# Optimization experiments

Measured on AMD Instinct MI355X. Metric: run time of the kernel, lower is better.

Reference implementation:

```python
import jax, jax.numpy as jnp
import numpy as np

N_NODES = 80000
N_EDGES = 1280000
IN_CH = 128
HID = 64
N_GRAPHS = 64
DROPOUT_P = 0.3


def setup_inputs() -> dict:
    key = jax.random.key(0)
    ks = jax.random.split(key, 12)
    x = jax.random.normal(ks[0], (N_NODES, IN_CH), dtype=jnp.float32)
    edge_index = jax.random.randint(ks[1], (2, N_EDGES), 0, N_NODES, dtype=jnp.int64 if jax.config.read('jax_enable_x64') else jnp.int32)
    batch = jnp.sort(jax.random.randint(ks[2], (N_NODES,), 0, N_GRAPHS))
    def lin(k, fan_in, fan_out):
        lim = 1.0 / np.sqrt(fan_in)
        kw, kb = jax.random.split(k)
        W = jax.random.uniform(kw, (fan_in, fan_out), minval=-lim, maxval=lim, dtype=jnp.float32)
        b = jax.random.uniform(kb, (fan_out,), minval=-lim, maxval=lim, dtype=jnp.float32)
        return W, b
    W1, b1 = lin(ks[3], IN_CH, HID)
    W2, b2 = lin(ks[4], HID, HID)
    W3, b3 = lin(ks[5], HID, HID)
    Wm1, bm1 = lin(ks[6], HID, HID)
    Wm2, bm2 = lin(ks[7], HID, 1)
    return {"x": x, "edge_index": edge_index, "batch": batch,
            "W1": W1, "b1": b1, "W2": W2, "b2": b2, "W3": W3, "b3": b3,
            "Wm1": Wm1, "bm1": bm1, "Wm2": Wm2, "bm2": bm2}


def _gcn_conv(x, W, b, src, dst, deg_inv_sqrt):
    # PyG GCNConv: h = X W; add self-loops; norm_e = d^-1/2[src] * d^-1/2[dst]
    h = x @ W  # [N, F]
    norm = deg_inv_sqrt[src] * deg_inv_sqrt[dst]  # [E]
    agg = jax.ops.segment_sum(h[src] * norm[:, None], dst, num_segments=x.shape[0])
    agg = agg + h * (deg_inv_sqrt * deg_inv_sqrt)[:, None]  # self-loop term d^-1
    return agg + b


def _dropout(x, key, p):
    keep = jax.random.bernoulli(key, 1.0 - p, x.shape)
    return jnp.where(keep, x / (1.0 - p), 0.0)


def reference(x, edge_index, batch, W1, b1, W2, b2, W3, b3, Wm1, bm1, Wm2, bm2):
    src, dst = edge_index[0], edge_index[1]
    N = x.shape[0]
    # in-degree on dst, +1 for self-loop (PyG default normalization)
    deg = jax.ops.segment_sum(jnp.ones_like(dst, dtype=x.dtype), dst, num_segments=N) + 1.0
    deg_inv_sqrt = jax.lax.rsqrt(deg)

    dk = jax.random.split(jax.random.key(42), 4)
    h = _dropout(jax.nn.relu(_gcn_conv(x, W1, b1, src, dst, deg_inv_sqrt)), dk[0], DROPOUT_P)
    h = _dropout(jax.nn.relu(_gcn_conv(h, W2, b2, src, dst, deg_inv_sqrt)), dk[1], DROPOUT_P)
    h = _dropout(jax.nn.relu(_gcn_conv(h, W3, b3, src, dst, deg_inv_sqrt)), dk[2], DROPOUT_P)

    # global mean pool per graph
    sums = jax.ops.segment_sum(h, batch, num_segments=N_GRAPHS)
    counts = jax.ops.segment_sum(jnp.ones((N,), dtype=h.dtype), batch, num_segments=N_GRAPHS)
    pooled = sums / jnp.maximum(counts, 1.0)[:, None]  # [G, HID]

    # MLP head: Linear -> ReLU -> Dropout -> Linear
    m = jax.nn.relu(pooled @ Wm1 + bm1)
    m = _dropout(m, dk[3], DROPOUT_P)
    return m @ Wm2 + bm2  # [G, 1]
```

## Files before the change

### kernel.cpp

```cpp
#include <hip/hip_runtime.h>
#include <hip/hip_fp8.h>
#include <stdint.h>

#define HID 64
#define INCH 128
#define NGRAPH 64
#define KEEPP 0.7f
#define CAP 64
#define CAPSH 6
#define BD 16

typedef __attribute__((ext_vector_type(8))) short short8;
typedef __attribute__((ext_vector_type(4))) float floatx4;

__device__ __forceinline__ uint8_t f2e4(float f) {
  __hip_fp8_e4m3 t(f);
  return (uint8_t)t.__x;
}
__device__ __forceinline__ float e42f(uint8_t b) {
  __hip_fp8_e4m3 t;
  t.__x = (__hip_fp8_storage_t)b;
  return (float)t;
}
__device__ __forceinline__ ushort f2bf(float v) {
  uint32_t u = __float_as_uint(v);
  return (ushort)((u + 0x7FFFu + ((u >> 16) & 1u)) >> 16);
}
__device__ __forceinline__ float bf2f(ushort b) {
  return __uint_as_float((uint32_t)b << 16);
}

__host__ __device__ inline void tf2x32(uint32_t k0, uint32_t k1,
                                       uint32_t& x0, uint32_t& x1) {
  const uint32_t ks2 = k0 ^ k1 ^ 0x1BD11BDAu;
#define ROTL32(v, d) (((v) << (d)) | ((v) >> (32 - (d))))
#define TF_RND(r) { x0 += x1; x1 = ROTL32(x1, r); x1 ^= x0; }
  x0 += k0; x1 += k1;
  TF_RND(13) TF_RND(15) TF_RND(26) TF_RND(6)
  x0 += k1;  x1 += ks2 + 1u;
  TF_RND(17) TF_RND(29) TF_RND(16) TF_RND(24)
  x0 += ks2; x1 += k0 + 2u;
  TF_RND(13) TF_RND(15) TF_RND(26) TF_RND(6)
  x0 += k0;  x1 += k1 + 3u;
  TF_RND(17) TF_RND(29) TF_RND(16) TF_RND(24)
  x0 += k1;  x1 += ks2 + 4u;
  TF_RND(13) TF_RND(15) TF_RND(26) TF_RND(6)
  x0 += ks2; x1 += k0 + 5u;
#undef TF_RND
#undef ROTL32
}

__device__ __forceinline__ bool keep_mask(uint32_t k0, uint32_t k1, uint32_t idx) {
  uint32_t x0 = 0u, x1 = idx;
  tf2x32(k0, k1, x0, x1);
  uint32_t bits = x0 ^ x1;
  float u = __uint_as_float((bits >> 9) | 0x3f800000u) - 1.0f;
  return u < KEEPP;
}

__device__ __forceinline__ void wsplit_one(const float* __restrict__ W,
                                           short8* __restrict__ Wh,
                                           short8* __restrict__ Wl, int i) {
  int lane = i & 63, f = i >> 6;
  int kc = f >> 2, ct = f & 3;
  int kbase = kc * 32 + ((lane >> 4) << 3);
  int n = ct * 16 + (lane & 15);
  short8 h, l;
#pragma unroll
  for (int j = 0; j < 8; ++j) {
    float w = W[(size_t)(kbase + j) * HID + n];
    uint32_t u = __float_as_uint(w);
    h[j] = (short)(u >> 16);
    float r = w - __uint_as_float(u & 0xFFFF0000u);
    l[j] = (short)(__float_as_uint(r) >> 16);
  }
  Wh[i] = h;
  Wl[i] = l;
}

__global__ __launch_bounds__(256) void k_w1(const float* __restrict__ W1,
                                            short8* __restrict__ Wh1,
                                            short8* __restrict__ Wl1) {
  wsplit_one(W1, Wh1, Wl1, blockIdx.x * 256 + (int)threadIdx.x);
}

template <int K, int OUTMODE>
__device__ __forceinline__ void mgemm_tile(const float* __restrict__ A,
                                           const short8* __restrict__ Wh,
                                           const short8* __restrict__ Wl,
                                           uint8_t* __restrict__ C,
                                           const int* __restrict__ counts,
                                           int N, int tile) {
  constexpr int KC = K / 32;
  const int lane = threadIdx.x & 63;
  const int wv = threadIdx.x >> 6;
  const int m = lane & 15;
  const int q = lane >> 4;
  const int row0 = tile * 64 + wv * 16;
  if (row0 >= N) return;
  const int arow = min(row0 + m, N - 1);
  const float* __restrict__ ap = A + (size_t)arow * K + (q << 3);

  floatx4 acc[4];
#pragma unroll
  for (int ct = 0; ct < 4; ++ct) acc[ct] = (floatx4){0.f, 0.f, 0.f, 0.f};

#pragma unroll
  for (int kc = 0; kc < KC; ++kc) {
    const floatx4* apv = (const floatx4*)(ap + kc * 32);
    floatx4 x0 = apv[0];
    floatx4 x1 = apv[1];
    short8 ah, al;
#pragma unroll
    for (int j = 0; j < 4; ++j) {
      uint32_t u = __float_as_uint(x0[j]);
      ah[j] = (short)(u >> 16);
      float r = x0[j] - __uint_as_float(u & 0xFFFF0000u);
      al[j] = (short)(__float_as_uint(r) >> 16);
    }
#pragma unroll
    for (int j = 0; j < 4; ++j) {
      uint32_t u = __float_as_uint(x1[j]);
      ah[4 + j] = (short)(u >> 16);
      float r = x1[j] - __uint_as_float(u & 0xFFFF0000u);
      al[4 + j] = (short)(__float_as_uint(r) >> 16);
    }
#pragma unroll
    for (int ct = 0; ct < 4; ++ct) {
      short8 bh = Wh[(kc * 4 + ct) * 64 + lane];
      short8 bl = Wl[(kc * 4 + ct) * 64 + lane];
      acc[ct] = __builtin_amdgcn_mfma_f32_16x16x32_bf16(ah, bh, acc[ct], 0, 0, 0);
      acc[ct] = __builtin_amdgcn_mfma_f32_16x16x32_bf16(ah, bl, acc[ct], 0, 0, 0);
      acc[ct] = __builtin_amdgcn_mfma_f32_16x16x32_bf16(al, bh, acc[ct], 0, 0, 0);
    }
  }

  if (OUTMODE == 0) {
    ushort* __restrict__ cp = (ushort*)C + (size_t)row0 * HID;
#pragma unroll
    for (int ct = 0; ct < 4; ++ct)
#pragma unroll
      for (int r = 0; r < 4; ++r) {
        int rr = (q << 2) + r;
        if (row0 + rr < N) cp[(size_t)rr * HID + ct * 16 + m] = f2bf(acc[ct][r]);
      }
  } else {
    float dv[4];
#pragma unroll
    for (int r = 0; r < 4; ++r) {
      int gr = min(row0 + (q << 2) + r, N - 1);
      dv[r] = rsqrtf((float)counts[gr] + 1.0f);
    }
    uint8_t* __restrict__ cp = C + (size_t)row0 * HID;
#pragma unroll
    for (int ct = 0; ct < 4; ++ct)
#pragma unroll
      for (int r = 0; r < 4; ++r) {
        int rr = (q << 2) + r;
        if (row0 + rr < N) cp[(size_t)rr * HID + ct * 16 + m] = f2e4(acc[ct][r] * dv[r]);
      }
  }
}

template <int K>
__global__ __launch_bounds__(256) void k_build_gemm(
    const float* __restrict__ A, const short8* __restrict__ Wh,
    const short8* __restrict__ Wl, uint8_t* __restrict__ C, int N,
    const int* __restrict__ src, const int* __restrict__ dst,
    int* __restrict__ counts, int* __restrict__ cap,
    int E, int build_blocks, int gemm_blocks,
    const float* __restrict__ W2, short8* __restrict__ Wh2, short8* __restrict__ Wl2,
    const float* __restrict__ W3, short8* __restrict__ Wh3, short8* __restrict__ Wl3,
    const int* __restrict__ batch, int* __restrict__ gends) {
  const int TB = build_blocks + gemm_blocks;
  const int tid = (int)threadIdx.x;
  if ((int)blockIdx.x >= TB) {
    int xb = (int)blockIdx.x - TB;
    if (xb < 2) {
      wsplit_one(W2, Wh2, Wl2, xb * 256 + tid);
    } else if (xb < 4) {
      wsplit_one(W3, Wh3, Wl3, (xb - 2) * 256 + tid);
    } else {
      int bi = xb - 4;
      for (int i = bi * 256 + tid; i < N; i += BD * 256) {
        int g = batch[i];
        int gn = (i + 1 < N) ? batch[i + 1] : -1;
        if (g != gn) gends[g] = i + 1;
      }
    }
    return;
  }
  const long T = (long)TB;
  const long b = (long)blockIdx.x;
  const long gb = (b * gemm_blocks) / T;
  const bool is_g = (((b + 1) * gemm_blocks) / T) != gb;
  if (!is_g) {
    int bb = (int)(b - gb);
    int e = bb * 256 + tid;
    if (e < E) {
      int s = src[e], d = dst[e];
      int r = atomicAdd(&counts[d], 1);
      if (r < CAP) cap[(d << CAPSH) + r] = s;
    }
    return;
  }
  mgemm_tile<K, 0>(A, Wh, Wl, C, nullptr, N, (int)gb);
}

template <int K>
__global__ __launch_bounds__(256) void k_mgemm_s(const float* __restrict__ A,
                                                 const short8* __restrict__ Wh,
                                                 const short8* __restrict__ Wl,
                                                 uint8_t* __restrict__ C,
                                                 const int* __restrict__ counts,
                                                 int N) {
  mgemm_tile<K, 1>(A, Wh, Wl, C, counts, N, (int)blockIdx.x);
}

__global__ __launch_bounds__(256) void k_scale(const ushort* __restrict__ Bh,
                                               const int* __restrict__ counts,
                                               uint8_t* __restrict__ B0, int N) {
  int t = blockIdx.x * 256 + threadIdx.x;
  int total = N * (HID / 8);
  if (t >= total) return;
  int node = t >> 3;
  float dn = rsqrtf((float)counts[node] + 1.0f);
  const ushort* ip = Bh + (size_t)t * 8;
  ushort4 a = *(const ushort4*)ip;
  ushort4 b = *(const ushort4*)(ip + 4);
  uint8_t o[8];
  o[0] = f2e4(bf2f(a.x) * dn); o[1] = f2e4(bf2f(a.y) * dn);
  o[2] = f2e4(bf2f(a.z) * dn); o[3] = f2e4(bf2f(a.w) * dn);
  o[4] = f2e4(bf2f(b.x) * dn); o[5] = f2e4(bf2f(b.y) * dn);
  o[6] = f2e4(bf2f(b.z) * dn); o[7] = f2e4(bf2f(b.w) * dn);
  *(uint2*)(B0 + (size_t)t * 8) = *(uint2*)o;
}

__global__ __launch_bounds__(256) void k_gather_s(const uint8_t* __restrict__ tmp,
                                                  const int* __restrict__ counts,
                                                  const int* __restrict__ cap,
                                                  const float* __restrict__ bias,
                                                  float* __restrict__ outh, int N,
                                                  uint32_t k0, uint32_t k1) {
  const int node = blockIdx.x * 4 + (threadIdx.x >> 6);
  const int lane = threadIdx.x & 63;
  if (node >= N) return;
  const int degn = __builtin_amdgcn_readfirstlane(counts[node]);
  const int deg = min(degn, CAP);
  const int base = node << CAPSH;
  const int idx = node * HID + lane;
  const float selfv = e42f(tmp[idx]);
  const float blane = bias[lane];
  float acc0 = 0.0f, acc1 = 0.0f, acc2 = 0.0f, acc3 = 0.0f;
  int j = 0;
  for (; j + 7 < deg; j += 8) {
    int4 e0 = *(const int4*)&cap[base + j];
    int4 e1 = *(const int4*)&cap[base + j + 4];
    float v0 = e42f(tmp[(size_t)e0.x * HID + lane]);
    float v1 = e42f(tmp[(size_t)e0.y * HID + lane]);
    float v2 = e42f(tmp[(size_t)e0.z * HID + lane]);
    float v3 = e42f(tmp[(size_t)e0.w * HID + lane]);
    float v4 = e42f(tmp[(size_t)e1.x * HID + lane]);
    float v5 = e42f(tmp[(size_t)e1.y * HID + lane]);
    float v6 = e42f(tmp[(size_t)e1.z * HID + lane]);
    float v7 = e42f(tmp[(size_t)e1.w * HID + lane]);
    acc0 += v0; acc1 += v1; acc2 += v2; acc3 += v3;
    acc0 += v4; acc1 += v5; acc2 += v6; acc3 += v7;
  }
  for (; j + 1 < deg; j += 2) {
    int2 p = *(const int2*)&cap[base + j];
    acc0 += e42f(tmp[(size_t)p.x * HID + lane]);
    acc1 += e42f(tmp[(size_t)p.y * HID + lane]);
  }
  if (j < deg) {
    int s = cap[base + j];
    acc2 += e42f(tmp[(size_t)s * HID + lane]);
  }
  float acc = (acc0 + acc1) + (acc2 + acc3);
  const float dn = rsqrtf((float)degn + 1.0f);
  float v = dn * (acc + selfv) + blane;
  v = fmaxf(v, 0.0f);
  v = keep_mask(k0, k1, (uint32_t)idx) ? v / KEEPP : 0.0f;
  outh[idx] = v;
}

__global__ __launch_bounds__(256) void k_pool(const float* __restrict__ h,
                                              const int* __restrict__ batch,
                                              float* __restrict__ sums, int N) {
  __shared__ float ls[NGRAPH * HID];
  for (int i = threadIdx.x; i < NGRAPH * HID; i += 256) ls[i] = 0.0f;
  __syncthreads();
  const int lane = threadIdx.x & 63;
  const int wave = threadIdx.x >> 6;
  int per = (N + gridDim.x - 1) / gridDim.x;
  int beg = blockIdx.x * per;
  int end = min(N, beg + per);
  for (int i = beg + wave; i < end; i += 4) {
    int g = batch[i];
    atomicAdd(&ls[g * HID + lane], h[(size_t)i * HID + lane]);
  }
  __syncthreads();
  for (int i = threadIdx.x; i < NGRAPH * HID; i += 256)
    if (ls[i] != 0.0f) atomicAdd(&sums[i], ls[i]);
}

__global__ __launch_bounds__(256) void k_head(const float* __restrict__ sums,
                                              const int* __restrict__ gends,
                                              const float* __restrict__ Wm1,
                                              const float* __restrict__ bm1,
                                              const float* __restrict__ Wm2,
                                              const float* __restrict__ bm2,
                                              float* __restrict__ out,
                                              uint32_t k0, uint32_t k1) {
  __shared__ float cnts_s[NGRAPH];
  __shared__ float pooled[NGRAPH * HID];
  __shared__ float m[NGRAPH * HID];
  if (threadIdx.x < 64) {
    int g = threadIdx.x;
    int e = gends[g];
#pragma unroll
    for (int off = 1; off < 64; off <<= 1) {
      int o = __shfl_up(e, off);
      if (g >= off) e = max(e, o);
    }
    int prev = __shfl_up(e, 1);
    if (g == 0) prev = 0;
    cnts_s[g] = (float)(e - prev);
  }
  __syncthreads();
  for (int i = threadIdx.x; i < NGRAPH * HID; i += 256) {
    int g = i >> 6;
    pooled[i] = sums[i] / fmaxf(cnts_s[g], 1.0f);
  }
  __syncthreads();
  for (int i = threadIdx.x; i < NGRAPH * HID; i += 256) {
    int g = i >> 6, j = i & 63;
    float acc = bm1[j];
#pragma unroll 8
    for (int k = 0; k < HID; ++k)
      acc = fmaf(pooled[g * HID + k], Wm1[k * HID + j], acc);
    acc = fmaxf(acc, 0.0f);
    m[i] = keep_mask(k0, k1, (uint32_t)i) ? acc / KEEPP : 0.0f;
  }
  __syncthreads();
  if (threadIdx.x < NGRAPH) {
    int g = threadIdx.x;
    float acc = bm2[0];
#pragma unroll 8
    for (int j = 0; j < HID; ++j)
      acc = fmaf(m[g * HID + j], Wm2[j], acc);
    out[g] = acc;
  }
}

extern "C" void kernel_launch(void* const* d_in, const int* in_sizes, int n_in,
                              void* d_out, int out_size, void* d_ws, size_t ws_size,
                              hipStream_t stream) {
  const float* x     = (const float*)d_in[0];
  const int*   ei    = (const int*)d_in[1];
  const int*   batch = (const int*)d_in[2];
  const float* W1 = (const float*)d_in[3];
  const float* b1 = (const float*)d_in[4];
  const float* W2 = (const float*)d_in[5];
  const float* b2 = (const float*)d_in[6];
  const float* W3 = (const float*)d_in[7];
  const float* b3 = (const float*)d_in[8];
  const float* Wm1 = (const float*)d_in[9];
  const float* bm1 = (const float*)d_in[10];
  const float* Wm2 = (const float*)d_in[11];
  const float* bm2 = (const float*)d_in[12];
  float* out = (float*)d_out;

  const int N = in_sizes[0] / INCH;
  const int E = in_sizes[1] / 2;
  const int* src = ei;
  const int* dst = ei + E;

  char* ws = (char*)d_ws;
  size_t off = 0;
  uint8_t* B0 = (uint8_t*)(ws + off); off += (size_t)N * HID;
  off = (off + 15) & ~(size_t)15;
  float* B1     = (float*)(ws + off); off += (size_t)N * HID * 4;
  int*   counts = (int*)  (ws + off); off += (size_t)N * 4;
  float* sums   = (float*)(ws + off); off += NGRAPH * HID * 4;
  int*   gends  = (int*)  (ws + off); off += NGRAPH * 4;
  int*   cap    = (int*)  (ws + off); off += (size_t)N * CAP * 4;
  off = (off + 15) & ~(size_t)15;
  short8* Wh1 = (short8*)(ws + off); off += 1024 * 16;
  short8* Wl1 = (short8*)(ws + off); off += 1024 * 16;
  short8* Wh2 = (short8*)(ws + off); off += 512 * 16;
  short8* Wl2 = (short8*)(ws + off); off += 512 * 16;
  short8* Wh3 = (short8*)(ws + off); off += 512 * 16;
  short8* Wl3 = (short8*)(ws + off); off += 512 * 16;
  ushort* Bh = (ushort*)B1;

  uint32_t dk[4][2];
  for (uint32_t i = 0; i < 4; ++i) {
    uint32_t a = 0u, b = i;
    tf2x32(0u, 42u, a, b);
    dk[i][0] = a; dk[i][1] = b;
  }

  const int build_grid = (E + 255) / 256;
  const int mg_grid    = (N + 63) / 64;
  const int gath_grid  = (N + 3) / 4;
  const int scale_grid = (N * (HID / 8) + 255) / 256;

  hipMemsetAsync(counts, 0, (size_t)N * 4 + NGRAPH * HID * 4 + NGRAPH * 4, stream);
  k_w1<<<4, 256, 0, stream>>>(W1, Wh1, Wl1);

  k_build_gemm<INCH><<<build_grid + mg_grid + 4 + BD, 256, 0, stream>>>(
      x, Wh1, Wl1, (uint8_t*)Bh, N, src, dst, counts, cap, E,
      build_grid, mg_grid, W2, Wh2, Wl2, W3, Wh3, Wl3, batch, gends);
  k_scale<<<scale_grid, 256, 0, stream>>>(Bh, counts, B0, N);
  k_gather_s<<<gath_grid, 256, 0, stream>>>(B0, counts, cap, b1,
                                            B1, N, dk[0][0], dk[0][1]);
  k_mgemm_s<HID><<<mg_grid, 256, 0, stream>>>(B1, Wh2, Wl2, B0, counts, N);
  k_gather_s<<<gath_grid, 256, 0, stream>>>(B0, counts, cap, b2,
                                            B1, N, dk[1][0], dk[1][1]);
  k_mgemm_s<HID><<<mg_grid, 256, 0, stream>>>(B1, Wh3, Wl3, B0, counts, N);
  k_gather_s<<<gath_grid, 256, 0, stream>>>(B0, counts, cap, b3,
                                            B1, N, dk[2][0], dk[2][1]);

  k_pool<<<256, 256, 0, stream>>>(B1, batch, sums, N);
  k_head<<<1, 256, 0, stream>>>(sums, gends, Wm1, bm1, Wm2, bm2, out,
                                dk[3][0], dk[3][1]);
  (void)n_in; (void)out_size; (void)ws_size;
}
```

Before: 370.3 us.

## Store layer activations as bf16 and vectorize neighbor gather over 4-byte fp8 loads

Intermediate activations between layers are now written as bf16 instead of fp32. The layer-2/3 GEMMs read bf16 directly and drop the lo-part MFMA on A, and pooling reads bf16. The gather kernel is restructured so each 16-lane subgroup handles one neighbor with 4-byte fp8 loads, reduced with cross-lane shuffles. This cuts memory traffic and the number of gather load instructions, at the cost of bf16 rounding on activations and extra shuffle work.

```diff
diff --git a/kernel.cpp b/kernel.cpp
--- a/kernel.cpp
+++ b/kernel.cpp
@@ -84,13 +84,12 @@
   wsplit_one(W1, Wh1, Wl1, blockIdx.x * 256 + (int)threadIdx.x);
 }
 
-template <int K, int OUTMODE>
-__device__ __forceinline__ void mgemm_tile(const float* __restrict__ A,
-                                           const short8* __restrict__ Wh,
-                                           const short8* __restrict__ Wl,
-                                           uint8_t* __restrict__ C,
-                                           const int* __restrict__ counts,
-                                           int N, int tile) {
+template <int K>
+__device__ __forceinline__ void mgemm_tile_f32(const float* __restrict__ A,
+                                               const short8* __restrict__ Wh,
+                                               const short8* __restrict__ Wl,
+                                               ushort* __restrict__ C,
+                                               int N, int tile) {
   constexpr int KC = K / 32;
   const int lane = threadIdx.x & 63;
   const int wv = threadIdx.x >> 6;
@@ -135,37 +134,20 @@
     }
   }
 
-  if (OUTMODE == 0) {
-    ushort* __restrict__ cp = (ushort*)C + (size_t)row0 * HID;
-#pragma unroll
-    for (int ct = 0; ct < 4; ++ct)
-#pragma unroll
-      for (int r = 0; r < 4; ++r) {
-        int rr = (q << 2) + r;
-        if (row0 + rr < N) cp[(size_t)rr * HID + ct * 16 + m] = f2bf(acc[ct][r]);
-      }
-  } else {
-    float dv[4];
+  ushort* __restrict__ cp = C + (size_t)row0 * HID;
+#pragma unroll
+  for (int ct = 0; ct < 4; ++ct)
 #pragma unroll
     for (int r = 0; r < 4; ++r) {
-      int gr = min(row0 + (q << 2) + r, N - 1);
-      dv[r] = rsqrtf((float)counts[gr] + 1.0f);
-    }
-    uint8_t* __restrict__ cp = C + (size_t)row0 * HID;
-#pragma unroll
-    for (int ct = 0; ct < 4; ++ct)
-#pragma unroll
-      for (int r = 0; r < 4; ++r) {
-        int rr = (q << 2) + r;
-        if (row0 + rr < N) cp[(size_t)rr * HID + ct * 16 + m] = f2e4(acc[ct][r] * dv[r]);
-      }
-  }
+      int rr = (q << 2) + r;
+      if (row0 + rr < N) cp[(size_t)rr * HID + ct * 16 + m] = f2bf(acc[ct][r]);
+    }
 }
 
 template <int K>
 __global__ __launch_bounds__(256) void k_build_gemm(
     const float* __restrict__ A, const short8* __restrict__ Wh,
-    const short8* __restrict__ Wl, uint8_t* __restrict__ C, int N,
+    const short8* __restrict__ Wl, ushort* __restrict__ C, int N,
     const int* __restrict__ src, const int* __restrict__ dst,
     int* __restrict__ counts, int* __restrict__ cap,
     int E, int build_blocks, int gemm_blocks,
@@ -204,17 +186,56 @@
     }
     return;
   }
-  mgemm_tile<K, 0>(A, Wh, Wl, C, nullptr, N, (int)gb);
+  mgemm_tile_f32<K>(A, Wh, Wl, C, N, (int)gb);
 }
 
 template <int K>
-__global__ __launch_bounds__(256) void k_mgemm_s(const float* __restrict__ A,
+__global__ __launch_bounds__(256) void k_mgemm_b(const ushort* __restrict__ A,
                                                  const short8* __restrict__ Wh,
                                                  const short8* __restrict__ Wl,
                                                  uint8_t* __restrict__ C,
                                                  const int* __restrict__ counts,
                                                  int N) {
-  mgemm_tile<K, 1>(A, Wh, Wl, C, counts, N, (int)blockIdx.x);
+  constexpr int KC = K / 32;
+  const int lane = threadIdx.x & 63;
+  const int wv = threadIdx.x >> 6;
+  const int m = lane & 15;
+  const int q = lane >> 4;
+  const int row0 = (int)blockIdx.x * 64 + wv * 16;
+  if (row0 >= N) return;
+  const int arow = min(row0 + m, N - 1);
+  const ushort* __restrict__ ap = A + (size_t)arow * K + (q << 3);
+
+  floatx4 acc[4];
+#pragma unroll
+  for (int ct = 0; ct < 4; ++ct) acc[ct] = (floatx4){0.f, 0.f, 0.f, 0.f};
+
+#pragma unroll
+  for (int kc = 0; kc < KC; ++kc) {
+    short8 ah = *(const short8*)(ap + kc * 32);
+#pragma unroll
+    for (int ct = 0; ct < 4; ++ct) {
+      short8 bh = Wh[(kc * 4 + ct) * 64 + lane];
+      short8 bl = Wl[(kc * 4 + ct) * 64 + lane];
+      acc[ct] = __builtin_amdgcn_mfma_f32_16x16x32_bf16(ah, bh, acc[ct], 0, 0, 0);
+      acc[ct] = __builtin_amdgcn_mfma_f32_16x16x32_bf16(ah, bl, acc[ct], 0, 0, 0);
+    }
+  }
+
+  float dv[4];
+#pragma unroll
+  for (int r = 0; r < 4; ++r) {
+    int gr = min(row0 + (q << 2) + r, N - 1);
+    dv[r] = rsqrtf((float)counts[gr] + 1.0f);
+  }
+  uint8_t* __restrict__ cp = C + (size_t)row0 * HID;
+#pragma unroll
+  for (int ct = 0; ct < 4; ++ct)
+#pragma unroll
+    for (int r = 0; r < 4; ++r) {
+      int rr = (q << 2) + r;
+      if (row0 + rr < N) cp[(size_t)rr * HID + ct * 16 + m] = f2e4(acc[ct][r] * dv[r]);
+    }
 }
 
 __global__ __launch_bounds__(256) void k_scale(const ushort* __restrict__ Bh,
@@ -240,7 +261,7 @@
                                                   const int* __restrict__ counts,
                                                   const int* __restrict__ cap,
                                                   const float* __restrict__ bias,
-                                                  float* __restrict__ outh, int N,
+                                                  ushort* __restrict__ outh, int N,
                                                   uint32_t k0, uint32_t k1) {
   const int node = blockIdx.x * 4 + (threadIdx.x >> 6);
   const int lane = threadIdx.x & 63;
@@ -251,40 +272,53 @@
   const int idx = node * HID + lane;
   const float selfv = e42f(tmp[idx]);
   const float blane = bias[lane];
-  float acc0 = 0.0f, acc1 = 0.0f, acc2 = 0.0f, acc3 = 0.0f;
-  int j = 0;
-  for (; j + 7 < deg; j += 8) {
-    int4 e0 = *(const int4*)&cap[base + j];
-    int4 e1 = *(const int4*)&cap[base + j + 4];
-    float v0 = e42f(tmp[(size_t)e0.x * HID + lane]);
-    float v1 = e42f(tmp[(size_t)e0.y * HID + lane]);
-    float v2 = e42f(tmp[(size_t)e0.z * HID + lane]);
-    float v3 = e42f(tmp[(size_t)e0.w * HID + lane]);
-    float v4 = e42f(tmp[(size_t)e1.x * HID + lane]);
-    float v5 = e42f(tmp[(size_t)e1.y * HID + lane]);
-    float v6 = e42f(tmp[(size_t)e1.z * HID + lane]);
-    float v7 = e42f(tmp[(size_t)e1.w * HID + lane]);
-    acc0 += v0; acc1 += v1; acc2 += v2; acc3 += v3;
-    acc0 += v4; acc1 += v5; acc2 += v6; acc3 += v7;
-  }
-  for (; j + 1 < deg; j += 2) {
-    int2 p = *(const int2*)&cap[base + j];
-    acc0 += e42f(tmp[(size_t)p.x * HID + lane]);
-    acc1 += e42f(tmp[(size_t)p.y * HID + lane]);
-  }
-  if (j < deg) {
-    int s = cap[base + j];
-    acc2 += e42f(tmp[(size_t)s * HID + lane]);
-  }
-  float acc = (acc0 + acc1) + (acc2 + acc3);
+  const int sub = lane >> 4;
+  const int ch4 = (lane & 15) << 2;
+  float a0 = 0.0f, a1 = 0.0f, a2 = 0.0f, a3 = 0.0f;
+  for (int j = 0; j < deg; j += 8) {
+    int4 ea = *(const int4*)&cap[base + j];
+    int4 eb = *(const int4*)&cap[base + j + 4];
+    int sa = (sub & 1) ? ea.y : ea.x;
+    int ta = (sub & 1) ? ea.w : ea.z;
+    sa = (sub & 2) ? ta : sa;
+    int sb = (sub & 1) ? eb.y : eb.x;
+    int tb = (sub & 1) ? eb.w : eb.z;
+    sb = (sub & 2) ? tb : sb;
+    uint32_t wa = 0u, wb = 0u;
+    if (j + sub < deg)
+      wa = *(const uint32_t*)(tmp + ((size_t)sa << 6) + ch4);
+    if (j + 4 + sub < deg)
+      wb = *(const uint32_t*)(tmp + ((size_t)sb << 6) + ch4);
+    a0 += e42f((uint8_t)(wa & 255u));
+    a1 += e42f((uint8_t)((wa >> 8) & 255u));
+    a2 += e42f((uint8_t)((wa >> 16) & 255u));
+    a3 += e42f((uint8_t)(wa >> 24));
+    a0 += e42f((uint8_t)(wb & 255u));
+    a1 += e42f((uint8_t)((wb >> 8) & 255u));
+    a2 += e42f((uint8_t)((wb >> 16) & 255u));
+    a3 += e42f((uint8_t)(wb >> 24));
+  }
+  a0 += __shfl_xor(a0, 16); a1 += __shfl_xor(a1, 16);
+  a2 += __shfl_xor(a2, 16); a3 += __shfl_xor(a3, 16);
+  a0 += __shfl_xor(a0, 32); a1 += __shfl_xor(a1, 32);
+  a2 += __shfl_xor(a2, 32); a3 += __shfl_xor(a3, 32);
+  const int srcl = lane >> 2;
+  float t0 = __shfl(a0, srcl);
+  float t1 = __shfl(a1, srcl);
+  float t2 = __shfl(a2, srcl);
+  float t3 = __shfl(a3, srcl);
+  float u01 = (lane & 1) ? t1 : t0;
+  float u23 = (lane & 1) ? t3 : t2;
+  float acc = (lane & 2) ? u23 : u01;
+
   const float dn = rsqrtf((float)degn + 1.0f);
   float v = dn * (acc + selfv) + blane;
   v = fmaxf(v, 0.0f);
   v = keep_mask(k0, k1, (uint32_t)idx) ? v / KEEPP : 0.0f;
-  outh[idx] = v;
-}
-
-__global__ __launch_bounds__(256) void k_pool(const float* __restrict__ h,
+  outh[idx] = f2bf(v);
+}
+
+__global__ __launch_bounds__(256) void k_pool(const ushort* __restrict__ h,
                                               const int* __restrict__ batch,
                                               float* __restrict__ sums, int N) {
   __shared__ float ls[NGRAPH * HID];
@@ -297,7 +331,7 @@
   int end = min(N, beg + per);
   for (int i = beg + wave; i < end; i += 4) {
     int g = batch[i];
-    atomicAdd(&ls[g * HID + lane], h[(size_t)i * HID + lane]);
+    atomicAdd(&ls[g * HID + lane], bf2f(h[(size_t)i * HID + lane]));
   }
   __syncthreads();
   for (int i = threadIdx.x; i < NGRAPH * HID; i += 256)
@@ -380,7 +414,7 @@
   size_t off = 0;
   uint8_t* B0 = (uint8_t*)(ws + off); off += (size_t)N * HID;
   off = (off + 15) & ~(size_t)15;
-  float* B1     = (float*)(ws + off); off += (size_t)N * HID * 4;
+  ushort* B1    = (ushort*)(ws + off); off += (size_t)N * HID * 2;
   int*   counts = (int*)  (ws + off); off += (size_t)N * 4;
   float* sums   = (float*)(ws + off); off += NGRAPH * HID * 4;
   int*   gends  = (int*)  (ws + off); off += NGRAPH * 4;
@@ -392,7 +426,7 @@
   short8* Wl2 = (short8*)(ws + off); off += 512 * 16;
   short8* Wh3 = (short8*)(ws + off); off += 512 * 16;
   short8* Wl3 = (short8*)(ws + off); off += 512 * 16;
-  ushort* Bh = (ushort*)B1;
+  ushort* Bh = B1;
 
   uint32_t dk[4][2];
   for (uint32_t i = 0; i < 4; ++i) {
@@ -410,15 +444,15 @@
   k_w1<<<4, 256, 0, stream>>>(W1, Wh1, Wl1);
 
   k_build_gemm<INCH><<<build_grid + mg_grid + 4 + BD, 256, 0, stream>>>(
-      x, Wh1, Wl1, (uint8_t*)Bh, N, src, dst, counts, cap, E,
+      x, Wh1, Wl1, Bh, N, src, dst, counts, cap, E,
       build_grid, mg_grid, W2, Wh2, Wl2, W3, Wh3, Wl3, batch, gends);
   k_scale<<<scale_grid, 256, 0, stream>>>(Bh, counts, B0, N);
   k_gather_s<<<gath_grid, 256, 0, stream>>>(B0, counts, cap, b1,
                                             B1, N, dk[0][0], dk[0][1]);
-  k_mgemm_s<HID><<<mg_grid, 256, 0, stream>>>(B1, Wh2, Wl2, B0, counts, N);
+  k_mgemm_b<HID><<<mg_grid, 256, 0, stream>>>(B1, Wh2, Wl2, B0, counts, N);
   k_gather_s<<<gath_grid, 256, 0, stream>>>(B0, counts, cap, b2,
                                             B1, N, dk[1][0], dk[1][1]);
-  k_mgemm_s<HID><<<mg_grid, 256, 0, stream>>>(B1, Wh3, Wl3, B0, counts, N);
+  k_mgemm_b<HID><<<mg_grid, 256, 0, stream>>>(B1, Wh3, Wl3, B0, counts, N);
   k_gather_s<<<gath_grid, 256, 0, stream>>>(B0, counts, cap, b3,
                                             B1, N, dk[2][0], dk[2][1]);
 
```

Result: no change. 370.0 us (-0.1%).
